# Kernel tuning notes

Hardware: AMD Instinct MI355X
Metric: run time of the kernel (lower is better)

The kernel has to match this reference:

```python
import jax, jax.numpy as jnp
import numpy as np

B, T, D, H = 2, 2048, 1024, 16
DK = D // H

def setup_inputs() -> dict:
    key = jax.random.key(0)
    ks = jax.random.split(key, 12)
    s = 1.0 / np.sqrt(D)
    inp = {
        'Q': jax.random.normal(ks[0], (B, T, D), jnp.float32),
        'K': jax.random.normal(ks[1], (B, T, D), jnp.float32),
        'V': jax.random.normal(ks[2], (B, T, D), jnp.float32),
        'mask': jnp.tril(jnp.ones((T, T), jnp.int32))[None, None],  # causal [1,1,T,T]
        'Wq_w': jax.random.normal(ks[3], (D, D), jnp.float32) * s,
        'Wq_b': jax.random.normal(ks[4], (D,), jnp.float32) * s,
        'Wk_w': jax.random.normal(ks[5], (D, D), jnp.float32) * s,
        'Wk_b': jax.random.normal(ks[6], (D,), jnp.float32) * s,
        'Wv_w': jax.random.normal(ks[7], (D, D), jnp.float32) * s,
        'Wv_b': jax.random.normal(ks[8], (D,), jnp.float32) * s,
        'Wo_w': jax.random.normal(ks[9], (D, D), jnp.float32) * s,
        'Wo_b': jax.random.normal(ks[10], (D,), jnp.float32) * s,
    }
    return inp

def reference(Q, K, V, mask, Wq_w, Wq_b, Wk_w, Wk_b, Wv_w, Wv_b, Wo_w, Wo_b):
    b, tq, c = Q.shape
    tk = K.shape[1]
    q = (Q @ Wq_w + Wq_b).reshape(b, tq, H, DK).transpose(0, 2, 1, 3)  # [B,H,Tq,dk]
    k = (K @ Wk_w + Wk_b).reshape(b, tk, H, DK).transpose(0, 2, 1, 3)
    v = (V @ Wv_w + Wv_b).reshape(b, tk, H, DK).transpose(0, 2, 1, 3)
    scores = jnp.einsum('bhqd,bhkd->bhqk', q, k) / jnp.sqrt(jnp.float32(DK))
    scores = jnp.where(mask == 0, jnp.float32(-1e9), scores)
    attn = jax.nn.softmax(scores, axis=-1)
    out = jnp.einsum('bhqk,bhkd->bhqd', attn, v)
    out = out.transpose(0, 2, 1, 3).reshape(b, tq, c)
    return out @ Wo_w + Wo_b
```

## Files before the change

### kernel.cpp

```cpp
#include <hip/hip_runtime.h>
#include <hip/hip_bf16.h>

#define NB 2
#define NT 2048
#define ND 1024
#define NH 16
#define NDK 64

typedef __attribute__((ext_vector_type(8))) short bf16x8;
typedef __attribute__((ext_vector_type(4))) float f32x4;

static __device__ __forceinline__ short f2bf(float f) {
  union { float f; unsigned u; } c; c.f = f;
  unsigned u = c.u;
  u += 0x7FFF + ((u >> 16) & 1);
  return (short)(u >> 16);
}

static __device__ __forceinline__ unsigned cvt_pk_bf16(float lo, float hi) {
  unsigned r;
  asm("v_cvt_pk_bf16_f32 %0, %1, %2" : "=v"(r) : "v"(lo), "v"(hi));
  return r;
}

static __device__ __forceinline__ void gload16(const void* g, void* l) {
  __builtin_amdgcn_global_load_lds((const __attribute__((address_space(1))) void*)g,
                                   (__attribute__((address_space(3))) void*)l, 16, 0, 0);
}

__global__ void prep_kernel(const float* __restrict__ Q, const float* __restrict__ Ki,
                            const float* __restrict__ V,
                            short* __restrict__ Qb, short* __restrict__ Kb, short* __restrict__ Vb,
                            const float* __restrict__ W0, const float* __restrict__ W1,
                            const float* __restrict__ W2, const float* __restrict__ W3,
                            short* __restrict__ T0, short* __restrict__ T1,
                            short* __restrict__ T2, short* __restrict__ T3) {
  __shared__ float t[32][33];
  int d = blockIdx.x, tid = threadIdx.x;
  if (d < 6144) {
    int z = d >> 11;
    int i = (d & 2047) * 256 + tid;
    const float* src = z == 0 ? Q : (z == 1 ? Ki : V);
    short* dst       = z == 0 ? Qb : (z == 1 ? Kb : Vb);
    const float4* s4 = (const float4*)src + (size_t)i * 2;
    float4 a = s4[0], b = s4[1];
    bf16x8 o;
    o[0] = f2bf(a.x); o[1] = f2bf(a.y); o[2] = f2bf(a.z); o[3] = f2bf(a.w);
    o[4] = f2bf(b.x); o[5] = f2bf(b.y); o[6] = f2bf(b.z); o[7] = f2bf(b.w);
    *((bf16x8*)dst + i) = o;
  } else {
    int dd = d - 6144;
    int z = dd >> 10;
    int rem = dd & 1023;
    const float* W = z == 0 ? W0 : (z == 1 ? W1 : (z == 2 ? W2 : W3));
    short* Wt      = z == 0 ? T0 : (z == 1 ? T1 : (z == 2 ? T2 : T3));
    int n0 = (rem & 31) * 32, k0 = (rem >> 5) * 32;
    int tx = tid & 31, ty = tid >> 5;
    for (int i = ty; i < 32; i += 8) t[i][tx] = W[(size_t)(k0 + i) * ND + n0 + tx];
    __syncthreads();
    for (int i = ty; i < 32; i += 8) Wt[(size_t)(n0 + i) * ND + k0 + tx] = f2bf(t[tx][i]);
  }
}

template <int MODE, int BN>
__global__ __launch_bounds__(256, 3) void gemm_bt(
    const short* __restrict__ A0, const short* __restrict__ A1, const short* __restrict__ A2,
    const short* __restrict__ W0, const short* __restrict__ W1, const short* __restrict__ W2,
    const float* __restrict__ b0, const float* __restrict__ b1, const float* __restrict__ b2,
    void* o0, void* o1, void* o2)
{
  constexpr int K = ND;
  constexpr int NI = BN / 32;
  constexpr int NNB = ND / BN;
  constexpr int NZ = (MODE == 0) ? 3 : 1;
  constexpr int NWPX = NZ * 32 * NNB / 8;
  __shared__ short As[2][128 * 32];
  __shared__ short Bs[2][BN * 32];

  int d = blockIdx.x;
  int work = (d & 7) * NWPX + (d >> 3);
  int z = work / (32 * NNB);
  int rem = work % (32 * NNB);
  int m0 = (rem / NNB) * 128, n0 = (rem % NNB) * BN;

  const short* A    = z == 0 ? A0 : (z == 1 ? A1 : A2);
  const short* Wt   = z == 0 ? W0 : (z == 1 ? W1 : W2);
  const float* bias = z == 0 ? b0 : (z == 1 ? b1 : b2);
  void* out         = z == 0 ? o0 : (z == 1 ? o1 : o2);
  float scl = (MODE == 0 && z == 0) ? 0.18033688011112042f : 1.0f;

  int tid = threadIdx.x, wid = tid >> 6, lane = tid & 63;
  int wr = wid >> 1, wc = wid & 1;
  int r16 = lane & 15, l4 = lane >> 4;

  auto stage = [&](int buf, int kt) {
    int row = (lane >> 2);
    int c8 = (lane & 3) * 8;
    {
      int rbase = wid * 32;
      const short* ga = A + (size_t)(m0 + rbase + row) * K + kt * 32 + c8;
      gload16(ga,          &As[buf][rbase * 32]);
      gload16(ga + 16 * K, &As[buf][(rbase + 16) * 32]);
    }
    if constexpr (BN == 128) {
      int rbase = wid * 32;
      const short* gb = Wt + (size_t)(n0 + rbase + row) * K + kt * 32 + c8;
      gload16(gb,          &Bs[buf][rbase * 32]);
      gload16(gb + 16 * K, &Bs[buf][(rbase + 16) * 32]);
    } else {
      int rbase = wid * 16;
      const short* gb = Wt + (size_t)(n0 + rbase + row) * K + kt * 32 + c8;
      gload16(gb,          &Bs[buf][rbase * 32]);
    }
  };

  f32x4 acc[4][NI] = {};
  stage(0, 0);
  __syncthreads();

  for (int kt = 0; kt < K / 32; ++kt) {
    int cur = kt & 1;
    if (kt + 1 < K / 32) stage(cur ^ 1, kt + 1);
    bf16x8 af[4], bfv[NI];
    int kk = l4 * 8;
#pragma unroll
    for (int mi = 0; mi < 4; mi++)
      af[mi] = *(const bf16x8*)&As[cur][(wr * 64 + mi * 16 + r16) * 32 + kk];
#pragma unroll
    for (int ni = 0; ni < NI; ni++)
      bfv[ni] = *(const bf16x8*)&Bs[cur][(wc * (BN / 2) + ni * 16 + r16) * 32 + kk];
#pragma unroll
    for (int mi = 0; mi < 4; mi++)
#pragma unroll
      for (int ni = 0; ni < NI; ni++)
        acc[mi][ni] = __builtin_amdgcn_mfma_f32_16x16x32_bf16(af[mi], bfv[ni], acc[mi][ni], 0, 0, 0);
    __syncthreads();
  }

  int mb = m0 + wr * 64, nb = n0 + wc * (BN / 2);
#pragma unroll
  for (int mi = 0; mi < 4; mi++)
#pragma unroll
    for (int ni = 0; ni < NI; ni++) {
      int n = nb + ni * 16 + r16;
      float bv = bias[n];
      if constexpr (MODE == 0) {
        int h = n >> 6, dk = n & 63;
        if (z == 2) {
          int m0_ = mb + mi * 16 + l4 * 4;
          int bI = m0_ >> 11, t0 = m0_ & (NT - 1);
          int bh = bI * NH + h;
          short4 s4;
          s4.x = f2bf(acc[mi][ni][0] + bv);
          s4.y = f2bf(acc[mi][ni][1] + bv);
          s4.z = f2bf(acc[mi][ni][2] + bv);
          s4.w = f2bf(acc[mi][ni][3] + bv);
          *(short4*)&((short*)out)[(size_t)bh * 131072 + (dk >> 4) * 32768 +
                                   (t0 >> 3) * 128 + (dk & 15) * 8 + (t0 & 7)] = s4;
        } else if (z == 1) {
#pragma unroll
          for (int r = 0; r < 4; r++) {
            int m = mb + mi * 16 + l4 * 4 + r;
            int bI = m >> 11, t = m & (NT - 1);
            int bh = bI * NH + h;
            ((short*)out)[(size_t)bh * 131072 + (t >> 4) * 1024 + (dk >> 3) * 128 +
                          (t & 15) * 8 + (dk & 7)] = f2bf(acc[mi][ni][r] + bv);
          }
        } else {
#pragma unroll
          for (int r = 0; r < 4; r++) {
            int m = mb + mi * 16 + l4 * 4 + r;
            int bI = m >> 11, t = m & (NT - 1);
            ((short*)out)[((((size_t)bI * NH + h) * NT + t) << 6) + dk] = f2bf((acc[mi][ni][r] + bv) * scl);
          }
        }
      } else {
#pragma unroll
        for (int r = 0; r < 4; r++) {
          int m = mb + mi * 16 + l4 * 4 + r;
          ((float*)out)[(size_t)m * ND + n] = acc[mi][ni][r] + bv;
        }
      }
    }
}

__global__ __launch_bounds__(256) void attn_kernel(
    const short* __restrict__ q, const short* __restrict__ k, const short* __restrict__ vt,
    short* __restrict__ O)
{
  struct SH {
    union {
      short p2[4][2][16][72];
      struct {
        f32x4 obuf[4][2][2][64];
        float ol[4][32];
      } mg;
    };
  };
  __shared__ SH sh;

  int d = blockIdx.x;
  int xcd = d & 7, jj = d >> 3;
  int bh = xcd * 4 + (jj >> 5);
  int pair = jj & 31;
  int b = bh >> 4, h = bh & 15;
  int tid = threadIdx.x, wid = tid >> 6, lane = tid & 63;
  int r16 = lane & 15, l4 = lane >> 4;
  size_t hb = (size_t)bh * NT * NDK;
  const short* qh = q + hb;
  const short* kh = k + hb;
  const short* vh = vt + hb;

#pragma unroll 1
  for (int half = 0; half < 2; ++half) {
    int qg = half == 0 ? (63 - pair) : pair;
    int qw = qg * 32;

    bf16x8 qa[2][2];
#pragma unroll
    for (int rf = 0; rf < 2; rf++)
#pragma unroll
      for (int kf = 0; kf < 2; kf++)
        qa[rf][kf] = *(const bf16x8*)(qh + (size_t)(qw + rf * 16 + r16) * NDK + kf * 32 + l4 * 8);

    f32x4 of[2][4] = {};
    float l0 = 0.f, l1 = 0.f;

    int nt = (qw + 95) >> 6;

    bf16x8 kfr[4][2];
    if (wid < nt) {
#pragma unroll
      for (int cf = 0; cf < 4; cf++) {
        const short* kb_ = kh + (size_t)((wid * 64 >> 4) + cf) * 1024 + lane * 8;
        kfr[cf][0] = *(const bf16x8*)kb_;
        kfr[cf][1] = *(const bf16x8*)(kb_ + 512);
      }
    }

    for (int kt = wid; kt < nt; kt += 4) {
      int kv0 = kt * 64;

      bf16x8 vb[4][2];
#pragma unroll
      for (int df = 0; df < 4; df++)
#pragma unroll
        for (int kf = 0; kf < 2; kf++)
          vb[df][kf] = *(const bf16x8*)(vh + df * 32768 + (kv0 >> 3) * 128 + kf * 512 + lane * 8);

      f32x4 sf[2][4] = {};
#pragma unroll
      for (int cf = 0; cf < 4; cf++) {
        sf[0][cf] = __builtin_amdgcn_mfma_f32_16x16x32_bf16(kfr[cf][0], qa[0][0], sf[0][cf], 0, 0, 0);
        sf[0][cf] = __builtin_amdgcn_mfma_f32_16x16x32_bf16(kfr[cf][1], qa[0][1], sf[0][cf], 0, 0, 0);
      }
#pragma unroll
      for (int cf = 0; cf < 4; cf++) {
        sf[1][cf] = __builtin_amdgcn_mfma_f32_16x16x32_bf16(kfr[cf][0], qa[1][0], sf[1][cf], 0, 0, 0);
        sf[1][cf] = __builtin_amdgcn_mfma_f32_16x16x32_bf16(kfr[cf][1], qa[1][1], sf[1][cf], 0, 0, 0);
      }

      {
        int ktn = (kt + 4 < nt) ? kt + 4 : kt;
        int kvn = ktn * 64;
#pragma unroll
        for (int cf = 0; cf < 4; cf++) {
          const short* kb_ = kh + (size_t)((kvn >> 4) + cf) * 1024 + lane * 8;
          kfr[cf][0] = *(const bf16x8*)kb_;
          kfr[cf][1] = *(const bf16x8*)(kb_ + 512);
        }
      }

      bool nm = (kv0 + 63 > qw);

      if (nm) {
#pragma unroll
        for (int cf = 0; cf < 4; cf++)
#pragma unroll
          for (int r = 0; r < 4; r++) {
            int kvi = kv0 + cf * 16 + l4 * 4 + r;
            if (kvi > qw + r16) sf[0][cf][r] = -1e30f;
          }
      }
      {
        float rs = 0.f;
#pragma unroll
        for (int cf = 0; cf < 4; cf++) {
          float p0 = __builtin_amdgcn_exp2f(sf[0][cf][0]);
          float p1 = __builtin_amdgcn_exp2f(sf[0][cf][1]);
          float p2v = __builtin_amdgcn_exp2f(sf[0][cf][2]);
          float p3 = __builtin_amdgcn_exp2f(sf[0][cf][3]);
          rs += (p0 + p1) + (p2v + p3);
          unsigned w0 = cvt_pk_bf16(p0, p1);
          unsigned w1 = cvt_pk_bf16(p2v, p3);
          *(int2*)&sh.p2[wid][0][r16][cf * 16 + l4 * 4] = make_int2((int)w0, (int)w1);
        }
        l0 += rs;
      }
#pragma unroll
      for (int kf = 0; kf < 2; kf++) {
        bf16x8 pa = *(const bf16x8*)&sh.p2[wid][0][r16][kf * 32 + l4 * 8];
#pragma unroll
        for (int df = 0; df < 4; df++)
          of[0][df] = __builtin_amdgcn_mfma_f32_16x16x32_bf16(vb[df][kf], pa, of[0][df], 0, 0, 0);
      }

      if (nm) {
#pragma unroll
        for (int cf = 0; cf < 4; cf++)
#pragma unroll
          for (int r = 0; r < 4; r++) {
            int kvi = kv0 + cf * 16 + l4 * 4 + r;
            if (kvi > qw + 16 + r16) sf[1][cf][r] = -1e30f;
          }
      }
      {
        float rs = 0.f;
#pragma unroll
        for (int cf = 0; cf < 4; cf++) {
          float p0 = __builtin_amdgcn_exp2f(sf[1][cf][0]);
          float p1 = __builtin_amdgcn_exp2f(sf[1][cf][1]);
          float p2v = __builtin_amdgcn_exp2f(sf[1][cf][2]);
          float p3 = __builtin_amdgcn_exp2f(sf[1][cf][3]);
          rs += (p0 + p1) + (p2v + p3);
          unsigned w0 = cvt_pk_bf16(p0, p1);
          unsigned w1 = cvt_pk_bf16(p2v, p3);
          *(int2*)&sh.p2[wid][1][r16][cf * 16 + l4 * 4] = make_int2((int)w0, (int)w1);
        }
        l1 += rs;
      }
#pragma unroll
      for (int kf = 0; kf < 2; kf++) {
        bf16x8 pa = *(const bf16x8*)&sh.p2[wid][1][r16][kf * 32 + l4 * 8];
#pragma unroll
        for (int df = 0; df < 4; df++)
          of[1][df] = __builtin_amdgcn_mfma_f32_16x16x32_bf16(vb[df][kf], pa, of[1][df], 0, 0, 0);
      }
    }

    l0 += __shfl_xor(l0, 16); l0 += __shfl_xor(l0, 32);
    l1 += __shfl_xor(l1, 16); l1 += __shfl_xor(l1, 32);

    __syncthreads();
    if (l4 == 0) {
      sh.mg.ol[wid][r16] = l0;
      sh.mg.ol[wid][16 + r16] = l1;
    }
#pragma unroll
    for (int pass = 0; pass < 2; ++pass) {
#pragma unroll
      for (int rf = 0; rf < 2; rf++)
#pragma unroll
        for (int dfp = 0; dfp < 2; dfp++)
          sh.mg.obuf[wid][rf][dfp][lane] = of[rf][2 * pass + dfp];
      __syncthreads();
      {
        int mrf = wid >> 1, mdfp = wid & 1, mdf = 2 * pass + mdfp;
        int row = mrf * 16 + r16;
        float lst = sh.mg.ol[0][row] + sh.mg.ol[1][row] + sh.mg.ol[2][row] + sh.mg.ol[3][row];
        float rinv = 1.0f / lst;
        f32x4 o0 = sh.mg.obuf[0][mrf][mdfp][lane];
        f32x4 o1 = sh.mg.obuf[1][mrf][mdfp][lane];
        f32x4 o2 = sh.mg.obuf[2][mrf][mdfp][lane];
        f32x4 o3 = sh.mg.obuf[3][mrf][mdfp][lane];
        float v0 = (o0[0] + o1[0] + o2[0] + o3[0]) * rinv;
        float v1 = (o0[1] + o1[1] + o2[1] + o3[1]) * rinv;
        float v2 = (o0[2] + o1[2] + o2[2] + o3[2]) * rinv;
        float v3 = (o0[3] + o1[3] + o2[3] + o3[3]) * rinv;
        int t = qw + mrf * 16 + r16;
        *(int2*)&O[(size_t)(b * NT + t) * ND + h * 64 + mdf * 16 + l4 * 4] =
            make_int2((int)cvt_pk_bf16(v0, v1), (int)cvt_pk_bf16(v2, v3));
      }
      __syncthreads();
    }
  }
}

extern "C" void kernel_launch(void* const* d_in, const int* in_sizes, int n_in,
                              void* d_out, int out_size, void* d_ws, size_t ws_size,
                              hipStream_t stream)
{
  const float* Q  = (const float*)d_in[0];
  const float* Ki = (const float*)d_in[1];
  const float* V  = (const float*)d_in[2];
  const float* Wq = (const float*)d_in[4];  const float* bq = (const float*)d_in[5];
  const float* Wk = (const float*)d_in[6];  const float* bk = (const float*)d_in[7];
  const float* Wv = (const float*)d_in[8];  const float* bv = (const float*)d_in[9];
  const float* Wo = (const float*)d_in[10]; const float* bo = (const float*)d_in[11];

  short* ws = (short*)d_ws;
  const size_t M4 = (size_t)4 * 1024 * 1024;
  short* Qb  = ws;
  short* Kb  = ws + M4;
  short* Vb  = ws + 2 * M4;
  short* qp  = ws + 3 * M4;
  short* kp  = ws + 4 * M4;
  short* vtp = ws + 5 * M4;
  short* Wqt = ws + 6 * M4;
  short* Wkt = Wqt + 1024 * 1024;
  short* Wvt = Wkt + 1024 * 1024;
  short* Wot = Wvt + 1024 * 1024;
  short* Obuf = Qb;

  prep_kernel<<<10240, 256, 0, stream>>>(Q, Ki, V, Qb, Kb, Vb,
                                         Wq, Wk, Wv, Wo, Wqt, Wkt, Wvt, Wot);

  gemm_bt<0, 128><<<768, 256, 0, stream>>>(Qb, Kb, Vb, Wqt, Wkt, Wvt,
                                           bq, bk, bv, qp, kp, vtp);
  attn_kernel<<<1024, 256, 0, stream>>>(qp, kp, vtp, Obuf);
  gemm_bt<1, 64><<<512, 256, 0, stream>>>(Obuf, Obuf, Obuf, Wot, Wot, Wot,
                                          bo, bo, bo, d_out, d_out, d_out);
}
```

Baseline: 115.8 us.

## Restructure attention to share double-buffered K/V tiles in LDS across eight waves

The attention kernel moves from 1024 blocks of 4 waves (each wave owning different KV tiles with a cross-wave merge) to 256 blocks of 8 waves. Each wave now owns 16 query rows, and the whole block shares K/V tiles staged through a double-buffered LDS copy. This drops the per-wave global K/V loads and the final LDS reduction of partial outputs and row sums. The cost is a block-wide barrier every KV tile, waves idling on tiles past their causal limit, and fewer blocks (256) to fill the CUs.

```diff
diff --git a/kernel.cpp b/kernel.cpp
--- a/kernel.cpp
+++ b/kernel.cpp
@@ -184,25 +184,17 @@
     }
 }
 
-__global__ __launch_bounds__(256) void attn_kernel(
+__global__ __launch_bounds__(512) void attn_kernel(
     const short* __restrict__ q, const short* __restrict__ k, const short* __restrict__ vt,
     short* __restrict__ O)
 {
-  struct SH {
-    union {
-      short p2[4][2][16][72];
-      struct {
-        f32x4 obuf[4][2][2][64];
-        float ol[4][32];
-      } mg;
-    };
-  };
-  __shared__ SH sh;
+  __shared__ short kv_lds[2][8192];
+  __shared__ short p2[8][16][72];
 
   int d = blockIdx.x;
   int xcd = d & 7, jj = d >> 3;
-  int bh = xcd * 4 + (jj >> 5);
-  int pair = jj & 31;
+  int bh = xcd * 4 + (jj & 3);
+  int p = jj >> 2;
   int b = bh >> 4, h = bh & 15;
   int tid = threadIdx.x, wid = tid >> 6, lane = tid & 63;
   int r16 = lane & 15, l4 = lane >> 4;
@@ -211,167 +203,97 @@
   const short* kh = k + hb;
   const short* vh = vt + hb;
 
+  int vdf = tid >> 7;
+  int voff = (tid & 127) * 8;
+
 #pragma unroll 1
   for (int half = 0; half < 2; ++half) {
-    int qg = half == 0 ? (63 - pair) : pair;
-    int qw = qg * 32;
-
-    bf16x8 qa[2][2];
-#pragma unroll
-    for (int rf = 0; rf < 2; rf++)
-#pragma unroll
-      for (int kf = 0; kf < 2; kf++)
-        qa[rf][kf] = *(const bf16x8*)(qh + (size_t)(qw + rf * 16 + r16) * NDK + kf * 32 + l4 * 8);
-
-    f32x4 of[2][4] = {};
-    float l0 = 0.f, l1 = 0.f;
-
-    int nt = (qw + 95) >> 6;
-
-    bf16x8 kfr[4][2];
-    if (wid < nt) {
+    int qb = half == 0 ? (15 - p) : p;
+    int qw = qb * 128 + wid * 16;
+    int nt = 2 * qb + 2;
+
+    bf16x8 qa[2];
+#pragma unroll
+    for (int kf = 0; kf < 2; kf++)
+      qa[kf] = *(const bf16x8*)(qh + (size_t)(qw + r16) * NDK + kf * 32 + l4 * 8);
+
+    f32x4 of[4] = {};
+    float l_ = 0.f;
+
+    __syncthreads();
+    {
+      gload16(kh + (size_t)0 * 1024 + tid * 8, &kv_lds[0][tid * 8]);
+      gload16(vh + (size_t)vdf * 32768 + 0 * 128 + voff, &kv_lds[0][4096 + vdf * 1024 + voff]);
+    }
+
+    for (int kt = 0; kt < nt; ++kt) {
+      int buf = kt & 1;
+      int kv0 = kt * 64;
+      __syncthreads();
+      if (kt + 1 < nt) {
+        int kvn = kv0 + 64;
+        gload16(kh + (size_t)(kvn >> 4) * 1024 + tid * 8, &kv_lds[buf ^ 1][tid * 8]);
+        gload16(vh + (size_t)vdf * 32768 + (kvn >> 3) * 128 + voff,
+                &kv_lds[buf ^ 1][4096 + vdf * 1024 + voff]);
+      }
+      if (kv0 > qw + 15) continue;
+
+      f32x4 sf[4] = {};
 #pragma unroll
       for (int cf = 0; cf < 4; cf++) {
-        const short* kb_ = kh + (size_t)((wid * 64 >> 4) + cf) * 1024 + lane * 8;
-        kfr[cf][0] = *(const bf16x8*)kb_;
-        kfr[cf][1] = *(const bf16x8*)(kb_ + 512);
-      }
-    }
-
-    for (int kt = wid; kt < nt; kt += 4) {
-      int kv0 = kt * 64;
-
-      bf16x8 vb[4][2];
-#pragma unroll
-      for (int df = 0; df < 4; df++)
-#pragma unroll
-        for (int kf = 0; kf < 2; kf++)
-          vb[df][kf] = *(const bf16x8*)(vh + df * 32768 + (kv0 >> 3) * 128 + kf * 512 + lane * 8);
-
-      f32x4 sf[2][4] = {};
-#pragma unroll
-      for (int cf = 0; cf < 4; cf++) {
-        sf[0][cf] = __builtin_amdgcn_mfma_f32_16x16x32_bf16(kfr[cf][0], qa[0][0], sf[0][cf], 0, 0, 0);
-        sf[0][cf] = __builtin_amdgcn_mfma_f32_16x16x32_bf16(kfr[cf][1], qa[0][1], sf[0][cf], 0, 0, 0);
-      }
-#pragma unroll
-      for (int cf = 0; cf < 4; cf++) {
-        sf[1][cf] = __builtin_amdgcn_mfma_f32_16x16x32_bf16(kfr[cf][0], qa[1][0], sf[1][cf], 0, 0, 0);
-        sf[1][cf] = __builtin_amdgcn_mfma_f32_16x16x32_bf16(kfr[cf][1], qa[1][1], sf[1][cf], 0, 0, 0);
-      }
-
-      {
-        int ktn = (kt + 4 < nt) ? kt + 4 : kt;
-        int kvn = ktn * 64;
-#pragma unroll
-        for (int cf = 0; cf < 4; cf++) {
-          const short* kb_ = kh + (size_t)((kvn >> 4) + cf) * 1024 + lane * 8;
-          kfr[cf][0] = *(const bf16x8*)kb_;
-          kfr[cf][1] = *(const bf16x8*)(kb_ + 512);
-        }
-      }
-
-      bool nm = (kv0 + 63 > qw);
-
-      if (nm) {
+        bf16x8 k0 = *(const bf16x8*)&kv_lds[buf][cf * 1024 + lane * 8];
+        bf16x8 k1 = *(const bf16x8*)&kv_lds[buf][cf * 1024 + 512 + lane * 8];
+        sf[cf] = __builtin_amdgcn_mfma_f32_16x16x32_bf16(k0, qa[0], sf[cf], 0, 0, 0);
+        sf[cf] = __builtin_amdgcn_mfma_f32_16x16x32_bf16(k1, qa[1], sf[cf], 0, 0, 0);
+      }
+
+      if (kv0 + 63 > qw) {
 #pragma unroll
         for (int cf = 0; cf < 4; cf++)
 #pragma unroll
           for (int r = 0; r < 4; r++) {
             int kvi = kv0 + cf * 16 + l4 * 4 + r;
-            if (kvi > qw + r16) sf[0][cf][r] = -1e30f;
+            if (kvi > qw + r16) sf[cf][r] = -1e30f;
           }
       }
+
       {
         float rs = 0.f;
 #pragma unroll
         for (int cf = 0; cf < 4; cf++) {
-          float p0 = __builtin_amdgcn_exp2f(sf[0][cf][0]);
-          float p1 = __builtin_amdgcn_exp2f(sf[0][cf][1]);
-          float p2v = __builtin_amdgcn_exp2f(sf[0][cf][2]);
-          float p3 = __builtin_amdgcn_exp2f(sf[0][cf][3]);
+          float p0 = __builtin_amdgcn_exp2f(sf[cf][0]);
+          float p1 = __builtin_amdgcn_exp2f(sf[cf][1]);
+          float p2v = __builtin_amdgcn_exp2f(sf[cf][2]);
+          float p3 = __builtin_amdgcn_exp2f(sf[cf][3]);
           rs += (p0 + p1) + (p2v + p3);
           unsigned w0 = cvt_pk_bf16(p0, p1);
           unsigned w1 = cvt_pk_bf16(p2v, p3);
-          *(int2*)&sh.p2[wid][0][r16][cf * 16 + l4 * 4] = make_int2((int)w0, (int)w1);
+          *(int2*)&p2[wid][r16][cf * 16 + l4 * 4] = make_int2((int)w0, (int)w1);
         }
-        l0 += rs;
-      }
+        l_ += rs;
+      }
+
 #pragma unroll
       for (int kf = 0; kf < 2; kf++) {
-        bf16x8 pa = *(const bf16x8*)&sh.p2[wid][0][r16][kf * 32 + l4 * 8];
-#pragma unroll
-        for (int df = 0; df < 4; df++)
-          of[0][df] = __builtin_amdgcn_mfma_f32_16x16x32_bf16(vb[df][kf], pa, of[0][df], 0, 0, 0);
-      }
-
-      if (nm) {
-#pragma unroll
-        for (int cf = 0; cf < 4; cf++)
-#pragma unroll
-          for (int r = 0; r < 4; r++) {
-            int kvi = kv0 + cf * 16 + l4 * 4 + r;
-            if (kvi > qw + 16 + r16) sf[1][cf][r] = -1e30f;
-          }
-      }
-      {
-        float rs = 0.f;
-#pragma unroll
-        for (int cf = 0; cf < 4; cf++) {
-          float p0 = __builtin_amdgcn_exp2f(sf[1][cf][0]);
-          float p1 = __builtin_amdgcn_exp2f(sf[1][cf][1]);
-          float p2v = __builtin_amdgcn_exp2f(sf[1][cf][2]);
-          float p3 = __builtin_amdgcn_exp2f(sf[1][cf][3]);
-          rs += (p0 + p1) + (p2v + p3);
-          unsigned w0 = cvt_pk_bf16(p0, p1);
-          unsigned w1 = cvt_pk_bf16(p2v, p3);
-          *(int2*)&sh.p2[wid][1][r16][cf * 16 + l4 * 4] = make_int2((int)w0, (int)w1);
+        bf16x8 pa = *(const bf16x8*)&p2[wid][r16][kf * 32 + l4 * 8];
+#pragma unroll
+        for (int df = 0; df < 4; df++) {
+          bf16x8 vf = *(const bf16x8*)&kv_lds[buf][4096 + df * 1024 + kf * 512 + lane * 8];
+          of[df] = __builtin_amdgcn_mfma_f32_16x16x32_bf16(vf, pa, of[df], 0, 0, 0);
         }
-        l1 += rs;
-      }
-#pragma unroll
-      for (int kf = 0; kf < 2; kf++) {
-        bf16x8 pa = *(const bf16x8*)&sh.p2[wid][1][r16][kf * 32 + l4 * 8];
-#pragma unroll
-        for (int df = 0; df < 4; df++)
-          of[1][df] = __builtin_amdgcn_mfma_f32_16x16x32_bf16(vb[df][kf], pa, of[1][df], 0, 0, 0);
-      }
-    }
-
-    l0 += __shfl_xor(l0, 16); l0 += __shfl_xor(l0, 32);
-    l1 += __shfl_xor(l1, 16); l1 += __shfl_xor(l1, 32);
-
-    __syncthreads();
-    if (l4 == 0) {
-      sh.mg.ol[wid][r16] = l0;
-      sh.mg.ol[wid][16 + r16] = l1;
-    }
-#pragma unroll
-    for (int pass = 0; pass < 2; ++pass) {
-#pragma unroll
-      for (int rf = 0; rf < 2; rf++)
-#pragma unroll
-        for (int dfp = 0; dfp < 2; dfp++)
-          sh.mg.obuf[wid][rf][dfp][lane] = of[rf][2 * pass + dfp];
-      __syncthreads();
-      {
-        int mrf = wid >> 1, mdfp = wid & 1, mdf = 2 * pass + mdfp;
-        int row = mrf * 16 + r16;
-        float lst = sh.mg.ol[0][row] + sh.mg.ol[1][row] + sh.mg.ol[2][row] + sh.mg.ol[3][row];
-        float rinv = 1.0f / lst;
-        f32x4 o0 = sh.mg.obuf[0][mrf][mdfp][lane];
-        f32x4 o1 = sh.mg.obuf[1][mrf][mdfp][lane];
-        f32x4 o2 = sh.mg.obuf[2][mrf][mdfp][lane];
-        f32x4 o3 = sh.mg.obuf[3][mrf][mdfp][lane];
-        float v0 = (o0[0] + o1[0] + o2[0] + o3[0]) * rinv;
-        float v1 = (o0[1] + o1[1] + o2[1] + o3[1]) * rinv;
-        float v2 = (o0[2] + o1[2] + o2[2] + o3[2]) * rinv;
-        float v3 = (o0[3] + o1[3] + o2[3] + o3[3]) * rinv;
-        int t = qw + mrf * 16 + r16;
-        *(int2*)&O[(size_t)(b * NT + t) * ND + h * 64 + mdf * 16 + l4 * 4] =
-            make_int2((int)cvt_pk_bf16(v0, v1), (int)cvt_pk_bf16(v2, v3));
-      }
-      __syncthreads();
+      }
+    }
+
+    l_ += __shfl_xor(l_, 16);
+    l_ += __shfl_xor(l_, 32);
+    float rinv = 1.0f / l_;
+    int t = qw + r16;
+#pragma unroll
+    for (int df = 0; df < 4; df++) {
+      unsigned w0 = cvt_pk_bf16(of[df][0] * rinv, of[df][1] * rinv);
+      unsigned w1 = cvt_pk_bf16(of[df][2] * rinv, of[df][3] * rinv);
+      *(int2*)&O[(size_t)(b * NT + t) * ND + h * 64 + df * 16 + l4 * 4] =
+          make_int2((int)w0, (int)w1);
     }
   }
 }
@@ -407,7 +329,7 @@
 
   gemm_bt<0, 128><<<768, 256, 0, stream>>>(Qb, Kb, Vb, Wqt, Wkt, Wvt,
                                            bq, bk, bv, qp, kp, vtp);
-  attn_kernel<<<1024, 256, 0, stream>>>(qp, kp, vtp, Obuf);
+  attn_kernel<<<256, 512, 0, stream>>>(qp, kp, vtp, Obuf);
   gemm_bt<1, 64><<<512, 256, 0, stream>>>(Obuf, Obuf, Obuf, Wot, Wot, Wot,
                                           bo, bo, bo, d_out, d_out, d_out);
 }
```

Result: slower. 119.7 us (+3.4%).
